# Kernel optimization log

Measured on AMD Instinct MI355X. Metric: run time of the kernel, lower is better.

Reference implementation:

```python
import jax, jax.numpy as jnp
import numpy as np

H = 16
D = 64  # head_dim = 1024 // 16
SCALE = D ** -0.5


def setup_inputs() -> dict:
    key = jax.random.key(0)
    ks = jax.random.split(key, 12)
    B, N, C = 2, 2048, 1024
    s = C ** -0.5
    return {
        "hidden_states": jax.random.normal(ks[0], (B, N, C), jnp.float32),
        "pos_embeds": jax.random.normal(ks[1], (B, N, C), jnp.float32),
        "Wq": jax.random.normal(ks[2], (C, C), jnp.float32) * s,
        "bq": jnp.zeros((C,), jnp.float32),
        "Wk": jax.random.normal(ks[3], (C, C), jnp.float32) * s,
        "bk": jnp.zeros((C,), jnp.float32),
        "Wv": jax.random.normal(ks[4], (C, C), jnp.float32) * s,
        "bv": jnp.zeros((C,), jnp.float32),
        "Wpos": jax.random.normal(ks[5], (C, C), jnp.float32) * s,
        "pos_bias_u": jax.random.normal(ks[6], (H, D), jnp.float32) * 0.1,
        "pos_bias_v": jax.random.normal(ks[7], (H, D), jnp.float32) * 0.1,
        "Wo": jax.random.normal(ks[8], (C, C), jnp.float32) * s,
        "bo": jnp.zeros((C,), jnp.float32),
    }


def reference(hidden_states, pos_embeds, Wq, bq, Wk, bk, Wv, bv, Wpos,
              pos_bias_u, pos_bias_v, Wo, bo):
    B, N, C = hidden_states.shape
    # projections (torch Linear: y = x @ W.T + b), split heads -> (B, N, H, D)
    q = (hidden_states @ Wq.T + bq).reshape(B, N, H, D)
    k = (hidden_states @ Wk.T + bk).reshape(B, N, H, D)
    v = (hidden_states @ Wv.T + bv).reshape(B, N, H, D)
    p = (pos_embeds @ Wpos.T).reshape(B, N, H, D)
    # relative-position biased logits: matrix_ac + matrix_bd
    q_u = q + pos_bias_u  # (B,N,H,D) + (H,D)
    q_v = q + pos_bias_v
    ac = jnp.einsum('bnhd,bmhd->bhnm', q_u, k)
    bd = jnp.einsum('bnhd,bmhd->bhnm', q_v, p)
    attn = jax.nn.softmax((ac + bd) * SCALE, axis=-1)  # (B,H,N,N)
    out = jnp.einsum('bhnm,bmhd->bnhd', attn, v).reshape(B, N, C)
    return out @ Wo.T + bo
```

## Files before the change

### kernel.cpp

```cpp
#include <hip/hip_runtime.h>
#include <hip/hip_bf16.h>


typedef short bf16x8 __attribute__((ext_vector_type(8)));
typedef float f32x4 __attribute__((ext_vector_type(4)));

#define BB 2
#define NN 2048
#define CC 1024
#define HH 16
#define DD 64
#define MM (BB * NN)
#define SC2E 0.18033688f

__device__ __forceinline__ unsigned short f2bf(float f) {
    union { float f; unsigned int u; } x; x.f = f;
    unsigned int r = x.u + 0x7FFFu + ((x.u >> 16) & 1u);
    return (unsigned short)(r >> 16);
}

__device__ __forceinline__ float bf2f(unsigned short s) {
    union { unsigned int u; float f; } x; x.u = ((unsigned int)s) << 16;
    return x.f;
}

__device__ __forceinline__ unsigned int pk2(float a, float b) {
    __hip_bfloat162 h = __float22bfloat162_rn(make_float2(a, b));
    unsigned int u; __builtin_memcpy(&u, &h, 4); return u;
}

typedef __attribute__((address_space(1))) const unsigned int* gas1_t;
typedef __attribute__((address_space(3))) unsigned int* las3_t;

__device__ __forceinline__ void gload_lds16(const unsigned short* g, unsigned short* l) {
    __builtin_amdgcn_global_load_lds((gas1_t)g, (las3_t)l, 16, 0, 0);
}

struct CastArgs {
    const float* src[7];
    unsigned short* dst[7];
    int n4[7];
};
__global__ __launch_bounds__(256) void cast_all(CastArgs a) {
    const int seg = blockIdx.y;
    const int i = blockIdx.x * 256 + threadIdx.x;
    if (i >= a.n4[seg]) return;
    float4 v = ((const float4*)a.src[seg])[i];
    uint2 u;
    u.x = pk2(v.x, v.y);
    u.y = pk2(v.z, v.w);
    ((uint2*)a.dst[seg])[i] = u;
}

struct GemmBatch {
    const unsigned short* A[4];
    const unsigned short* B[4];
    unsigned short* out[4];
    const float* bias[4];
};
__global__ __launch_bounds__(256) void gemm_qkvp(GemmBatch g) {
    constexpr int K = CC;
    __shared__ unsigned short Sh[2 * 128 * 64];
    unsigned short* As = Sh;
    unsigned short* Bs = Sh + 128 * 64;
    const int z = blockIdx.z;
    const unsigned short* __restrict__ A = g.A[z];
    const unsigned short* __restrict__ B = g.B[z];
    unsigned short* __restrict__ out = g.out[z];
    const float* __restrict__ bias = g.bias[z];

    const int t = threadIdx.x;
    const int w = t >> 6, lane = t & 63, l15 = lane & 15, quad = lane >> 4;
    const int m0 = blockIdx.x * 128, n0 = blockIdx.y * 128;
    const int wm = (w >> 1) * 64, wn = (w & 1) * 64;

    f32x4 acc[4][4];
#pragma unroll
    for (int i = 0; i < 4; ++i)
#pragma unroll
        for (int j = 0; j < 4; ++j)
#pragma unroll
            for (int r = 0; r < 4; ++r) acc[i][j][r] = 0.f;

    for (int kb = 0; kb < K; kb += 64) {
        __syncthreads();
#pragma unroll
        for (int j = 0; j < 4; ++j) {
            const int id = j * 256 + t;
            const int half = id >> 9;
            const int id9 = id & 511;
            const int row = id9 >> 2, c4 = (id9 & 3) * 8;
            gload_lds16(&A[(size_t)(m0 + row) * K + kb + half * 32 + c4],
                        &As[half * 4096 + id9 * 8]);
            gload_lds16(&B[(size_t)(n0 + row) * K + kb + half * 32 + c4],
                        &Bs[half * 4096 + id9 * 8]);
        }
        __syncthreads();
#pragma unroll
        for (int kk = 0; kk < 2; ++kk) {
            bf16x8 af[4], bfr[4];
#pragma unroll
            for (int i = 0; i < 4; ++i)
                af[i] = *(const bf16x8*)&As[kk * 4096 + (wm + i * 16 + l15) * 32 + quad * 8];
#pragma unroll
            for (int j = 0; j < 4; ++j)
                bfr[j] = *(const bf16x8*)&Bs[kk * 4096 + (wn + j * 16 + l15) * 32 + quad * 8];
#pragma unroll
            for (int i = 0; i < 4; ++i)
#pragma unroll
                for (int j = 0; j < 4; ++j)
                    acc[i][j] = __builtin_amdgcn_mfma_f32_16x16x32_bf16(af[i], bfr[j], acc[i][j], 0, 0, 0);
        }
    }

    if (z != 2) {
        const float sc = (z == 0) ? SC2E : 1.f;
#pragma unroll
        for (int i = 0; i < 4; ++i)
#pragma unroll
            for (int j = 0; j < 4; ++j) {
                const int col = n0 + wn + j * 16 + l15;
                const int row_base = m0 + wm + i * 16 + quad * 4;
                const float bc = bias ? bias[col] : 0.f;
#pragma unroll
                for (int r = 0; r < 4; ++r)
                    out[(size_t)(row_base + r) * CC + col] = f2bf((acc[i][j][r] + bc) * sc);
            }
    } else {
        __syncthreads();
        unsigned short* Tr = &Sh[w * 1152];
        const int bI = (m0 + wm) >> 11, nseq0 = (m0 + wm) & 2047;
        const int colL = lane >> 3;
        const int mL = (lane & 7) * 8;
#pragma unroll
        for (int j = 0; j < 4; ++j) {
            const int col = n0 + wn + j * 16 + l15;
            const float bc = bias[col];
#pragma unroll
            for (int i = 0; i < 4; ++i) {
                uint2 pk;
                pk.x = pk2(acc[i][j][0] + bc, acc[i][j][1] + bc);
                pk.y = pk2(acc[i][j][2] + bc, acc[i][j][3] + bc);
                *(uint2*)&Tr[l15 * 72 + i * 16 + quad * 4] = pk;
            }
#pragma unroll
            for (int p = 0; p < 2; ++p) {
                const int cl = p * 8 + colL;
                uint4 vv = *(const uint4*)&Tr[cl * 72 + mL];
                const int gcol = n0 + wn + j * 16 + cl;
                const int hh = gcol >> 6, dd = gcol & 63;
                *(uint4*)&out[((size_t)(bI * 16 + hh) * 64 + dd) * 2048 + nseq0 + mL] = vv;
            }
        }
    }
}

__global__ __launch_bounds__(256) void fuse_kpc(const unsigned short* __restrict__ k,
                                                const unsigned short* __restrict__ pp,
                                                const float* __restrict__ pbu,
                                                const float* __restrict__ pbv,
                                                unsigned short* __restrict__ kp,
                                                float* __restrict__ c) {
    const int gw = (blockIdx.x * 256 + threadIdx.x) >> 6;
    const int lane = threadIdx.x & 63;
    const int row = gw >> 4, h = gw & 15;
    const size_t off = (size_t)row * CC + h * 64 + lane;
    const float kv = bf2f(k[off]), pv = bf2f(pp[off]);
    kp[off] = f2bf(kv + pv);
    float val = pbu[h * 64 + lane] * kv + pbv[h * 64 + lane] * pv;
#pragma unroll
    for (int o = 1; o < 64; o <<= 1) val += __shfl_xor(val, o);
    if (lane == 0) {
        const int b = row >> 11, n = row & 2047;
        c[((size_t)(b * HH + h)) * NN + n] = val * SC2E;
    }
}

__global__ __launch_bounds__(512) void attn_kernel(const unsigned short* __restrict__ q,
                                                   const unsigned short* __restrict__ kp,
                                                   const unsigned short* __restrict__ vt,
                                                   const float* __restrict__ cb,
                                                   unsigned short* __restrict__ att) {
    __shared__ unsigned short Ks[2][128 * 64];
    __shared__ unsigned short Vs[2][64 * 128];
    __shared__ unsigned short Ps[8][16 * 64];

    const int t = threadIdx.x;
    const int w = t >> 6, lane = t & 63, l15 = lane & 15, quad = lane >> 4;
    const int qt = blockIdx.x, h = blockIdx.y, b = blockIdx.z;
    const int e3 = l15 & 7;

    bf16x8 qf[2];
    {
        const int qrow = qt * 128 + w * 16 + l15;
        const size_t qoff = ((size_t)(b * NN + qrow) * HH + h) * DD;
#pragma unroll
        for (int c2 = 0; c2 < 2; ++c2)
            qf[c2] = *(const bf16x8*)&q[qoff + c2 * 32 + quad * 8];
    }

    f32x4 oT[4];
    float l_lane = 0.f;
#pragma unroll
    for (int db = 0; db < 4; ++db)
#pragma unroll
        for (int r = 0; r < 4; ++r) oT[db][r] = 0.f;

    const size_t kbase = (size_t)b * NN * CC + (size_t)h * DD;
    const size_t vbase = (size_t)(b * HH + h) * DD * NN;
    const size_t cbase = (size_t)(b * HH + h) * NN;

    int krow[2], kgc[2], vd[2], vgc[2];
#pragma unroll
    for (int j = 0; j < 2; ++j) {
        const int id = j * 512 + t;
        krow[j] = id >> 3;
        kgc[j] = ((id & 7) ^ (krow[j] & 7)) * 8;
        vd[j] = id >> 4;
        vgc[j] = ((id & 15) ^ (vd[j] & 7)) * 8;
    }

#pragma unroll
    for (int j = 0; j < 2; ++j) {
        const int id = j * 512 + t;
        gload_lds16(&kp[kbase + (size_t)krow[j] * CC + kgc[j]], &Ks[0][id * 8]);
        gload_lds16(&vt[vbase + (size_t)vd[j] * NN + vgc[j]], &Vs[0][id * 8]);
    }

    for (int kt = 0; kt < NN / 128; ++kt) {
        const int cur = kt & 1;
        __syncthreads();
        if (kt + 1 < NN / 128) {
#pragma unroll
            for (int j = 0; j < 2; ++j) {
                const int id = j * 512 + t;
                gload_lds16(&kp[kbase + (size_t)((kt + 1) * 128 + krow[j]) * CC + kgc[j]],
                            &Ks[cur ^ 1][id * 8]);
                gload_lds16(&vt[vbase + (size_t)vd[j] * NN + (kt + 1) * 128 + vgc[j]],
                            &Vs[cur ^ 1][id * 8]);
            }
        }

        f32x4 c8r[8];
#pragma unroll
        for (int t8 = 0; t8 < 8; ++t8)
            c8r[t8] = *(const f32x4*)&cb[cbase + kt * 128 + t8 * 16 + quad * 4];

#pragma unroll
        for (int half = 0; half < 2; ++half) {
            f32x4 s[4];
#pragma unroll
            for (int t4 = 0; t4 < 4; ++t4) s[t4] = c8r[half * 4 + t4];

            __builtin_amdgcn_s_setprio(1);
#pragma unroll
            for (int t4 = 0; t4 < 4; ++t4) {
                const int row = half * 64 + t4 * 16 + l15;
#pragma unroll
                for (int c2 = 0; c2 < 2; ++c2) {
                    bf16x8 kf = *(const bf16x8*)&Ks[cur][row * 64 + (((c2 * 4 + quad) ^ e3) * 8)];
                    s[t4] = __builtin_amdgcn_mfma_f32_16x16x32_bf16(kf, qf[c2], s[t4], 0, 0, 0);
                }
            }
            __builtin_amdgcn_s_setprio(0);

            float rs = 0.f;
#pragma unroll
            for (int t4 = 0; t4 < 4; ++t4)
#pragma unroll
                for (int r = 0; r < 4; ++r) {
                    float pv = exp2f(s[t4][r]);
                    s[t4][r] = pv;
                    rs += pv;
                }
            l_lane += rs;
#pragma unroll
            for (int t4 = 0; t4 < 4; ++t4) {
                uint2 pk;
                pk.x = pk2(s[t4][0], s[t4][1]);
                pk.y = pk2(s[t4][2], s[t4][3]);
                const int blk = t4 * 2 + (quad >> 1);
                *(uint2*)&Ps[w][l15 * 64 + ((blk ^ e3) * 8) + (quad & 1) * 4] = pk;
            }

            __builtin_amdgcn_s_setprio(1);
#pragma unroll
            for (int c2 = 0; c2 < 2; ++c2) {
                bf16x8 pf = *(const bf16x8*)&Ps[w][l15 * 64 + (((c2 * 4 + quad) ^ e3) * 8)];
#pragma unroll
                for (int db = 0; db < 4; ++db) {
                    bf16x8 vf = *(const bf16x8*)&Vs[cur][(db * 16 + l15) * 128 +
                                                         (((half * 8 + c2 * 4 + quad) ^ e3) * 8)];
                    oT[db] = __builtin_amdgcn_mfma_f32_16x16x32_bf16(vf, pf, oT[db], 0, 0, 0);
                }
            }
            __builtin_amdgcn_s_setprio(0);
        }
    }

    float l = l_lane;
    l += __shfl_xor(l, 16);
    l += __shfl_xor(l, 32);
    const float inv = 1.f / l;
    const int qrow = qt * 128 + w * 16 + l15;
    const size_t ob = ((size_t)(b * NN + qrow) * HH + h) * DD;
#pragma unroll
    for (int db = 0; db < 4; ++db) {
        uint2 pk;
        pk.x = pk2(oT[db][0] * inv, oT[db][1] * inv);
        pk.y = pk2(oT[db][2] * inv, oT[db][3] * inv);
        *(uint2*)&att[ob + db * 16 + quad * 4] = pk;
    }
}

__global__ __launch_bounds__(256) void gemm_out(const unsigned short* __restrict__ A,
                                                const unsigned short* __restrict__ B,
                                                float* __restrict__ out,
                                                const float* __restrict__ bias) {
    constexpr int K = CC;
    __shared__ unsigned short As[128 * 32];
    __shared__ unsigned short Bs[64 * 32];
    const int t = threadIdx.x;
    const int w = t >> 6, lane = t & 63, l15 = lane & 15, quad = lane >> 4;
    const int m0 = blockIdx.x * 128, n0 = blockIdx.y * 64;
    const int wm = (w >> 1) * 64, wn = (w & 1) * 32;

    f32x4 acc[4][2];
#pragma unroll
    for (int i = 0; i < 4; ++i)
#pragma unroll
        for (int j = 0; j < 2; ++j)
#pragma unroll
            for (int r = 0; r < 4; ++r) acc[i][j][r] = 0.f;

    for (int kb = 0; kb < K; kb += 32) {
        __syncthreads();
#pragma unroll
        for (int j = 0; j < 2; ++j) {
            int id = j * 256 + t;
            int row = id >> 2, c4 = (id & 3) * 8;
            gload_lds16(&A[(size_t)(m0 + row) * K + kb + c4], &As[id * 8]);
        }
        {
            int row = t >> 2, c4 = (t & 3) * 8;
            gload_lds16(&B[(size_t)(n0 + row) * K + kb + c4], &Bs[t * 8]);
        }
        __syncthreads();
        bf16x8 af[4], bfr[2];
#pragma unroll
        for (int i = 0; i < 4; ++i)
            af[i] = *(const bf16x8*)&As[(wm + i * 16 + l15) * 32 + quad * 8];
#pragma unroll
        for (int j = 0; j < 2; ++j)
            bfr[j] = *(const bf16x8*)&Bs[(wn + j * 16 + l15) * 32 + quad * 8];
#pragma unroll
        for (int i = 0; i < 4; ++i)
#pragma unroll
            for (int j = 0; j < 2; ++j)
                acc[i][j] = __builtin_amdgcn_mfma_f32_16x16x32_bf16(af[i], bfr[j], acc[i][j], 0, 0, 0);
    }

#pragma unroll
    for (int i = 0; i < 4; ++i)
#pragma unroll
        for (int j = 0; j < 2; ++j) {
            const int col = n0 + wn + j * 16 + l15;
            const int row_base = m0 + wm + i * 16 + quad * 4;
            const float bc = bias[col];
#pragma unroll
            for (int r = 0; r < 4; ++r)
                out[(size_t)(row_base + r) * CC + col] = acc[i][j][r] + bc;
        }
}

extern "C" void kernel_launch(void* const* d_in, const int* in_sizes, int n_in,
                              void* d_out, int out_size, void* d_ws, size_t ws_size,
                              hipStream_t stream) {
    const float* hs   = (const float*)d_in[0];
    const float* pos  = (const float*)d_in[1];
    const float* Wq   = (const float*)d_in[2];
    const float* bq   = (const float*)d_in[3];
    const float* Wk   = (const float*)d_in[4];
    const float* bk   = (const float*)d_in[5];
    const float* Wv   = (const float*)d_in[6];
    const float* bv   = (const float*)d_in[7];
    const float* Wpos = (const float*)d_in[8];
    const float* pbu  = (const float*)d_in[9];
    const float* pbv  = (const float*)d_in[10];
    const float* Wo   = (const float*)d_in[11];
    const float* bo   = (const float*)d_in[12];
    float* out = (float*)d_out;

    const size_t nHS = (size_t)MM * CC;
    const size_t nW  = (size_t)CC * CC;

    unsigned short* p = (unsigned short*)d_ws;
    unsigned short* hsb  = p;            p += nHS;
    unsigned short* posb = p;            p += nHS;
    unsigned short* wqb  = p;            p += nW;
    unsigned short* wkb  = p;            p += nW;
    unsigned short* wvb  = p;            p += nW;
    unsigned short* wpb  = p;            p += nW;
    unsigned short* wob  = p;            p += nW;
    unsigned short* qsb  = p;            p += nHS;
    unsigned short* kbf  = p;            p += nHS;
    unsigned short* pbf  = p;            p += nHS;
    unsigned short* kpb  = p;            p += nHS;
    unsigned short* vtb  = p;            p += nHS;
    float* cb = (float*)p;               p += (size_t)BB * HH * NN * 2;
    unsigned short* attb = hsb;

    CastArgs ca;
    ca.src[0] = hs;   ca.dst[0] = hsb;  ca.n4[0] = (int)(nHS / 4);
    ca.src[1] = pos;  ca.dst[1] = posb; ca.n4[1] = (int)(nHS / 4);
    ca.src[2] = Wq;   ca.dst[2] = wqb;  ca.n4[2] = (int)(nW / 4);
    ca.src[3] = Wk;   ca.dst[3] = wkb;  ca.n4[3] = (int)(nW / 4);
    ca.src[4] = Wv;   ca.dst[4] = wvb;  ca.n4[4] = (int)(nW / 4);
    ca.src[5] = Wpos; ca.dst[5] = wpb;  ca.n4[5] = (int)(nW / 4);
    ca.src[6] = Wo;   ca.dst[6] = wob;  ca.n4[6] = (int)(nW / 4);
    dim3 cgrid((unsigned)(nHS / 4 / 256), 7);
    cast_all<<<cgrid, 256, 0, stream>>>(ca);

    GemmBatch gb;
    gb.A[0] = hsb;  gb.B[0] = wqb; gb.out[0] = qsb; gb.bias[0] = bq;
    gb.A[1] = hsb;  gb.B[1] = wkb; gb.out[1] = kbf; gb.bias[1] = bk;
    gb.A[2] = hsb;  gb.B[2] = wvb; gb.out[2] = vtb; gb.bias[2] = bv;
    gb.A[3] = posb; gb.B[3] = wpb; gb.out[3] = pbf; gb.bias[3] = nullptr;
    dim3 ggrid(MM / 128, CC / 128, 4);
    gemm_qkvp<<<ggrid, 256, 0, stream>>>(gb);

    fuse_kpc<<<MM * HH / 4, 256, 0, stream>>>(kbf, pbf, pbu, pbv, kpb, cb);

    dim3 agrid(NN / 128, HH, BB);
    attn_kernel<<<agrid, 512, 0, stream>>>(qsb, kpb, vtb, cb, attb);

    dim3 ogrid(MM / 128, CC / 64);
    gemm_out<<<ogrid, 256, 0, stream>>>(attb, wob, out, bo);
}
```

Measured before the change: 257.5 us.

## Fold K+P sum and bias-dot terms into a single concatenated-K GEMM

```diff
diff --git a/kernel.cpp b/kernel.cpp
--- a/kernel.cpp
+++ b/kernel.cpp
@@ -36,9 +36,36 @@
     __builtin_amdgcn_global_load_lds((gas1_t)g, (las3_t)l, 16, 0, 0);
 }
 
+__global__ __launch_bounds__(256) void compute_wuv(const float* __restrict__ Wk,
+                                                   const float* __restrict__ Wpos,
+                                                   const float* __restrict__ pbu,
+                                                   const float* __restrict__ pbv,
+                                                   const float* __restrict__ bk,
+                                                   unsigned short* __restrict__ wkpb,
+                                                   float* __restrict__ cub) {
+    const int gid = blockIdx.x * 256 + threadIdx.x;
+    const int h = gid >> 11;
+    const int col = gid & 2047;
+    const float* Wsrc = (col < 1024) ? Wk : Wpos;
+    const float* uv = (col < 1024) ? pbu : pbv;
+    const int c = col & 1023;
+    float acc = 0.f;
+#pragma unroll 8
+    for (int d = 0; d < 64; ++d)
+        acc += uv[h * 64 + d] * Wsrc[(size_t)(h * 64 + d) * 1024 + c];
+    wkpb[(size_t)(1024 + h) * 2048 + col] = f2bf(acc * SC2E);
+    if (gid < 16) {
+        float s = 0.f;
+        for (int d = 0; d < 64; ++d) s += pbu[gid * 64 + d] * bk[gid * 64 + d];
+        cub[gid] = s * SC2E;
+    }
+}
+
 struct CastArgs {
     const float* src[7];
     unsigned short* dst[7];
+    int stride[7];
+    int colOff[7];
     int n4[7];
 };
 __global__ __launch_bounds__(256) void cast_all(CastArgs a) {
@@ -49,25 +76,30 @@
     uint2 u;
     u.x = pk2(v.x, v.y);
     u.y = pk2(v.z, v.w);
-    ((uint2*)a.dst[seg])[i] = u;
+    const int row = i >> 8, c4 = (i & 255) * 4;
+    *(uint2*)&a.dst[seg][(size_t)row * a.stride[seg] + a.colOff[seg] + c4] = u;
 }
 
 struct GemmBatch {
-    const unsigned short* A[4];
-    const unsigned short* B[4];
-    unsigned short* out[4];
-    const float* bias[4];
+    const unsigned short* A[3];
+    const unsigned short* B[3];
+    unsigned short* out[3];
+    const float* bias[3];
+    int lda[3], ldb[3], Kz[3];
+    float* cbp;
+    const float* cub;
 };
 __global__ __launch_bounds__(256) void gemm_qkvp(GemmBatch g) {
-    constexpr int K = CC;
     __shared__ unsigned short Sh[2 * 128 * 64];
     unsigned short* As = Sh;
     unsigned short* Bs = Sh + 128 * 64;
     const int z = blockIdx.z;
+    if (z != 1 && blockIdx.y == 8) return;
     const unsigned short* __restrict__ A = g.A[z];
     const unsigned short* __restrict__ B = g.B[z];
     unsigned short* __restrict__ out = g.out[z];
     const float* __restrict__ bias = g.bias[z];
+    const int lda = g.lda[z], ldb = g.ldb[z], K = g.Kz[z];
 
     const int t = threadIdx.x;
     const int w = t >> 6, lane = t & 63, l15 = lane & 15, quad = lane >> 4;
@@ -90,9 +122,9 @@
             const int half = id >> 9;
             const int id9 = id & 511;
             const int row = id9 >> 2, c4 = (id9 & 3) * 8;
-            gload_lds16(&A[(size_t)(m0 + row) * K + kb + half * 32 + c4],
+            gload_lds16(&A[(size_t)(m0 + row) * lda + kb + half * 32 + c4],
                         &As[half * 4096 + id9 * 8]);
-            gload_lds16(&B[(size_t)(n0 + row) * K + kb + half * 32 + c4],
+            gload_lds16(&B[(size_t)(n0 + row) * ldb + kb + half * 32 + c4],
                         &Bs[half * 4096 + id9 * 8]);
         }
         __syncthreads();
@@ -113,7 +145,20 @@
         }
     }
 
-    if (z != 2) {
+    if (z == 1 && n0 == 1024) {
+        if ((w & 1) == 0) {
+            const int bI = (m0 + wm) >> 11;
+            const int nbase = (m0 + wm) & 2047;
+            const float cu = g.cub[l15];
+#pragma unroll
+            for (int i = 0; i < 4; ++i)
+#pragma unroll
+                for (int r = 0; r < 4; ++r) {
+                    const int nseq = nbase + i * 16 + quad * 4 + r;
+                    g.cbp[((size_t)(bI * 16 + l15)) * 2048 + nseq] = acc[i][0][r] + cu;
+                }
+        }
+    } else if (z != 2) {
         const float sc = (z == 0) ? SC2E : 1.f;
 #pragma unroll
         for (int i = 0; i < 4; ++i)
@@ -152,27 +197,6 @@
                 *(uint4*)&out[((size_t)(bI * 16 + hh) * 64 + dd) * 2048 + nseq0 + mL] = vv;
             }
         }
-    }
-}
-
-__global__ __launch_bounds__(256) void fuse_kpc(const unsigned short* __restrict__ k,
-                                                const unsigned short* __restrict__ pp,
-                                                const float* __restrict__ pbu,
-                                                const float* __restrict__ pbv,
-                                                unsigned short* __restrict__ kp,
-                                                float* __restrict__ c) {
-    const int gw = (blockIdx.x * 256 + threadIdx.x) >> 6;
-    const int lane = threadIdx.x & 63;
-    const int row = gw >> 4, h = gw & 15;
-    const size_t off = (size_t)row * CC + h * 64 + lane;
-    const float kv = bf2f(k[off]), pv = bf2f(pp[off]);
-    kp[off] = f2bf(kv + pv);
-    float val = pbu[h * 64 + lane] * kv + pbv[h * 64 + lane] * pv;
-#pragma unroll
-    for (int o = 1; o < 64; o <<= 1) val += __shfl_xor(val, o);
-    if (lane == 0) {
-        const int b = row >> 11, n = row & 2047;
-        c[((size_t)(b * HH + h)) * NN + n] = val * SC2E;
     }
 }
 
@@ -395,41 +419,38 @@
     const size_t nW  = (size_t)CC * CC;
 
     unsigned short* p = (unsigned short*)d_ws;
-    unsigned short* hsb  = p;            p += nHS;
-    unsigned short* posb = p;            p += nHS;
+    unsigned short* hspb = p;            p += (size_t)MM * 2048;
     unsigned short* wqb  = p;            p += nW;
-    unsigned short* wkb  = p;            p += nW;
+    unsigned short* wkpb = p;            p += (size_t)1152 * 2048;
     unsigned short* wvb  = p;            p += nW;
-    unsigned short* wpb  = p;            p += nW;
     unsigned short* wob  = p;            p += nW;
     unsigned short* qsb  = p;            p += nHS;
-    unsigned short* kbf  = p;            p += nHS;
-    unsigned short* pbf  = p;            p += nHS;
     unsigned short* kpb  = p;            p += nHS;
     unsigned short* vtb  = p;            p += nHS;
-    float* cb = (float*)p;               p += (size_t)BB * HH * NN * 2;
-    unsigned short* attb = hsb;
+    float* cb  = (float*)p;              p += (size_t)BB * HH * NN * 2;
+    float* cub = (float*)p;              p += 32;
+    unsigned short* attb = hspb;
+
+    compute_wuv<<<128, 256, 0, stream>>>(Wk, Wpos, pbu, pbv, bk, wkpb, cub);
 
     CastArgs ca;
-    ca.src[0] = hs;   ca.dst[0] = hsb;  ca.n4[0] = (int)(nHS / 4);
-    ca.src[1] = pos;  ca.dst[1] = posb; ca.n4[1] = (int)(nHS / 4);
-    ca.src[2] = Wq;   ca.dst[2] = wqb;  ca.n4[2] = (int)(nW / 4);
-    ca.src[3] = Wk;   ca.dst[3] = wkb;  ca.n4[3] = (int)(nW / 4);
-    ca.src[4] = Wv;   ca.dst[4] = wvb;  ca.n4[4] = (int)(nW / 4);
-    ca.src[5] = Wpos; ca.dst[5] = wpb;  ca.n4[5] = (int)(nW / 4);
-    ca.src[6] = Wo;   ca.dst[6] = wob;  ca.n4[6] = (int)(nW / 4);
+    ca.src[0] = hs;   ca.dst[0] = hspb; ca.stride[0] = 2048; ca.colOff[0] = 0;    ca.n4[0] = (int)(nHS / 4);
+    ca.src[1] = pos;  ca.dst[1] = hspb; ca.stride[1] = 2048; ca.colOff[1] = 1024; ca.n4[1] = (int)(nHS / 4);
+    ca.src[2] = Wq;   ca.dst[2] = wqb;  ca.stride[2] = 1024; ca.colOff[2] = 0;    ca.n4[2] = (int)(nW / 4);
+    ca.src[3] = Wk;   ca.dst[3] = wkpb; ca.stride[3] = 2048; ca.colOff[3] = 0;    ca.n4[3] = (int)(nW / 4);
+    ca.src[4] = Wpos; ca.dst[4] = wkpb; ca.stride[4] = 2048; ca.colOff[4] = 1024; ca.n4[4] = (int)(nW / 4);
+    ca.src[5] = Wv;   ca.dst[5] = wvb;  ca.stride[5] = 1024; ca.colOff[5] = 0;    ca.n4[5] = (int)(nW / 4);
+    ca.src[6] = Wo;   ca.dst[6] = wob;  ca.stride[6] = 1024; ca.colOff[6] = 0;    ca.n4[6] = (int)(nW / 4);
     dim3 cgrid((unsigned)(nHS / 4 / 256), 7);
     cast_all<<<cgrid, 256, 0, stream>>>(ca);
 
     GemmBatch gb;
-    gb.A[0] = hsb;  gb.B[0] = wqb; gb.out[0] = qsb; gb.bias[0] = bq;
-    gb.A[1] = hsb;  gb.B[1] = wkb; gb.out[1] = kbf; gb.bias[1] = bk;
-    gb.A[2] = hsb;  gb.B[2] = wvb; gb.out[2] = vtb; gb.bias[2] = bv;
-    gb.A[3] = posb; gb.B[3] = wpb; gb.out[3] = pbf; gb.bias[3] = nullptr;
-    dim3 ggrid(MM / 128, CC / 128, 4);
+    gb.A[0] = hspb; gb.lda[0] = 2048; gb.B[0] = wqb;  gb.ldb[0] = 1024; gb.Kz[0] = 1024; gb.out[0] = qsb; gb.bias[0] = bq;
+    gb.A[1] = hspb; gb.lda[1] = 2048; gb.B[1] = wkpb; gb.ldb[1] = 2048; gb.Kz[1] = 2048; gb.out[1] = kpb; gb.bias[1] = bk;
+    gb.A[2] = hspb; gb.lda[2] = 2048; gb.B[2] = wvb;  gb.ldb[2] = 1024; gb.Kz[2] = 1024; gb.out[2] = vtb; gb.bias[2] = bv;
+    gb.cbp = cb; gb.cub = cub;
+    dim3 ggrid(MM / 128, 9, 3);
     gemm_qkvp<<<ggrid, 256, 0, stream>>>(gb);
-
-    fuse_kpc<<<MM * HH / 4, 256, 0, stream>>>(kbf, pbf, pbu, pbv, kpb, cb);
 
     dim3 agrid(NN / 128, HH, BB);
     attn_kernel<<<agrid, 512, 0, stream>>>(qsb, kpb, vtb, cb, attb);
```

Result: slower. 267.1 us (+3.7%).
